# Kernel optimization log

Hardware: AMD Instinct MI355X
Metric: run time of the kernel (lower is better)

The kernel has to match this reference:

```python
import jax, jax.numpy as jnp
import numpy as np

N_NODES = 50000
N_EDGES = 1600000
IN_DIM, HID_DIM, OUT_DIM = 128, 256, 128


def setup_inputs() -> dict:
    key = jax.random.key(0)
    ks = jax.random.split(key, 8)
    x = jax.random.normal(ks[0], (N_NODES, IN_DIM), dtype=jnp.float32)
    edge_index = jax.random.randint(ks[1], (2, N_EDGES), 0, N_NODES, dtype=jnp.int64)
    s = 0.05
    # Layer 1: SAGEConv(IN_DIM -> HID_DIM); lin_l has bias, lin_r has no bias (PyG default)
    Wl1 = jax.random.normal(ks[2], (IN_DIM, HID_DIM), dtype=jnp.float32) * s
    bl1 = jnp.zeros((HID_DIM,), dtype=jnp.float32)
    Wr1 = jax.random.normal(ks[3], (IN_DIM, HID_DIM), dtype=jnp.float32) * s
    # Layer 2: SAGEConv(HID_DIM -> OUT_DIM)
    Wl2 = jax.random.normal(ks[4], (HID_DIM, OUT_DIM), dtype=jnp.float32) * s
    bl2 = jnp.zeros((OUT_DIM,), dtype=jnp.float32)
    Wr2 = jax.random.normal(ks[5], (HID_DIM, OUT_DIM), dtype=jnp.float32) * s
    return {"x": x, "edge_index": edge_index, "Wl1": Wl1, "bl1": bl1, "Wr1": Wr1,
            "Wl2": Wl2, "bl2": bl2, "Wr2": Wr2}


def _sage_conv(x, src, dst, Wl, bl, Wr, n_nodes):
    # mean aggregation of source-node features at destination nodes
    agg = jax.ops.segment_sum(x[src], dst, num_segments=n_nodes)  # [N, d_in]
    deg = jax.ops.segment_sum(jnp.ones_like(dst, dtype=x.dtype), dst, num_segments=n_nodes)
    mean = agg / jnp.maximum(deg, 1.0)[:, None]
    # out = lin_l(mean) + lin_r(x)
    return mean @ Wl + bl + x @ Wr


def reference(x, edge_index, Wl1, bl1, Wr1, Wl2, bl2, Wr2):
    src, dst = edge_index[0], edge_index[1]
    n = x.shape[0]
    h = _sage_conv(x, src, dst, Wl1, bl1, Wr1, n)
    h = jax.nn.relu(h)  # dropout is identity in eval mode
    out = _sage_conv(h, src, dst, Wl2, bl2, Wr2, n)
    return out
```

## Files before the change

kernel.cpp:

```cpp
#include <hip/hip_runtime.h>


#define IN_DIM 128
#define HID_DIM 256
#define OUT_DIM 128

#define EPB 8192
#define EPT 8
#define NBMAX 784
#define BCAP 4096

typedef unsigned short u16;
typedef unsigned int u32;
typedef unsigned char u8;
typedef __attribute__((ext_vector_type(8))) short short8;
typedef __attribute__((ext_vector_type(4))) float float4v;
typedef __attribute__((ext_vector_type(2))) float float2v;

#if defined(__has_builtin)
#if __has_builtin(__builtin_amdgcn_cvt_pk_f32_fp8) && \
    __has_builtin(__builtin_amdgcn_cvt_pk_fp8_f32)
#define HAVE_HW_FP8 1
#endif
#endif

static __device__ __forceinline__ u16 f2bf(float f) {
    u32 u = __builtin_bit_cast(u32, f);
    u = (u + 0x7fffu + ((u >> 16) & 1u)) >> 16;
    return (u16)u;
}
static __device__ __forceinline__ float bf2f(u32 lo16) {
    return __builtin_bit_cast(float, lo16 << 16);
}

#if !defined(HAVE_HW_FP8)
static __device__ __forceinline__ float fp8_dec1(u32 v) {
    u32 s = (v & 0x80u) << 24;
    u32 e = (v >> 3) & 0xFu;
    u32 m = v & 7u;
    float mag = e ? __builtin_bit_cast(float, ((e + 120u) << 23) | (m << 20))
                  : (float)m * 0x1p-9f;
    return __builtin_bit_cast(float, __builtin_bit_cast(u32, mag) | s);
}
static __device__ __forceinline__ u32 fp8_enc1(float f) {
    u32 u = __builtin_bit_cast(u32, f);
    u32 s = (u >> 24) & 0x80u;
    float af = fabsf(f);
    if (af > 448.f) af = 448.f;
    u32 a = __builtin_bit_cast(u32, af);
    int e = (int)((a >> 23) & 0xFF) - 127;
    u32 q;
    if (af < 0x1p-10f) q = 0;
    else if (e < -6) {
        q = (u32)__builtin_rintf(af * 512.f);
    } else {
        u32 m = a & 0x7FFFFFu;
        u32 r = m >> 20;
        u32 rem = m & 0xFFFFFu;
        if (rem > 0x80000u || (rem == 0x80000u && (r & 1u))) r++;
        u32 ee = (u32)(e + 7);
        if (r == 8u) { r = 0; ee++; }
        if (ee >= 16u) { ee = 15u; r = 6u; }
        q = (ee << 3) | r;
    }
    return s | q;
}
#endif

template <bool HI>
static __device__ __forceinline__ float2v fp8pk2f(u32 w) {
#if defined(HAVE_HW_FP8)
    return __builtin_amdgcn_cvt_pk_f32_fp8(w, HI);
#else
    float2v r;
    u32 b0 = HI ? ((w >> 16) & 0xFFu) : (w & 0xFFu);
    u32 b1 = HI ? (w >> 24) : ((w >> 8) & 0xFFu);
    r.x = fp8_dec1(b0);
    r.y = fp8_dec1(b1);
    return r;
#endif
}
template <bool HI>
static __device__ __forceinline__ u32 f2fp8pk(float a, float b, u32 old) {
#if defined(HAVE_HW_FP8)
    return (u32)__builtin_amdgcn_cvt_pk_fp8_f32(a, b, (int)old, HI);
#else
    u32 pk = fp8_enc1(a) | (fp8_enc1(b) << 8);
    return HI ? ((old & 0x0000FFFFu) | (pk << 16))
              : ((old & 0xFFFF0000u) | pk);
#endif
}
static __device__ __forceinline__ u8 f2fp8_1(float v) {
    return (u8)(f2fp8pk<false>(v, v, 0u) & 0xFFu);
}


__global__ __launch_bounds__(1024) void prep_part(
    const int* __restrict__ src, const int* __restrict__ dst, int n_edges,
    int nb, int nchunk, int* __restrict__ gcur, u32* __restrict__ pairs,
    const float* __restrict__ x, u16* __restrict__ xb, u32* __restrict__ xq,
    const float* __restrict__ Wl1, const float* __restrict__ Wr1,
    const float* __restrict__ Wl2, const float* __restrict__ Wr2,
    u16* __restrict__ WTl1, u16* __restrict__ WTr1,
    u16* __restrict__ WTl2, u16* __restrict__ WTr2, int n4, int xblocks) {
    __shared__ int h[NBMAX];
    __shared__ int curs[NBMAX];
    int b = blockIdx.x;
    int t = threadIdx.x;
    if (b < nchunk) {
        for (int i = t; i < nb; i += 1024) h[i] = 0;
        __syncthreads();
        int base = b * EPB;
        int dv[EPT], sv[EPT];
        bool on[EPT];
#pragma unroll
        for (int j = 0; j < EPT; j++) {
            int i = base + j * 1024 + t;
            on[j] = i < n_edges;
            if (on[j]) {
                dv[j] = dst[i];
                sv[j] = src[i];
                atomicAdd(&h[dv[j] >> 6], 1);
            }
        }
        __syncthreads();
        for (int i = t; i < nb; i += 1024) {
            int c = h[i];
            curs[i] = (c > 0) ? (i * BCAP + atomicAdd(&gcur[i], c)) : 0;
        }
        __syncthreads();
#pragma unroll
        for (int j = 0; j < EPT; j++) {
            if (on[j]) {
                int pos = atomicAdd(&curs[dv[j] >> 6], 1);
                pairs[pos] = ((u32)(dv[j] & 63) << 16) | (u32)sv[j];
            }
        }
        return;
    }
    if (b < nchunk + xblocks) {
        int i = (b - nchunk) * 1024 + t;
        if (i < n4) {
            float4 v = *(const float4*)(x + (size_t)i * 4);
            uint2 o;
            o.x = (u32)f2bf(v.x) | ((u32)f2bf(v.y) << 16);
            o.y = (u32)f2bf(v.z) | ((u32)f2bf(v.w) << 16);
            *(uint2*)(xb + (size_t)i * 4) = o;
            u32 q = f2fp8pk<false>(v.x, v.y, 0u);
            q = f2fp8pk<true>(v.z, v.w, q);
            xq[i] = q;
        }
        return;
    }
    int j = (b - nchunk - xblocks) * 1024 + t;
    if (j >= 4 * 32768) return;
    int seg = j >> 15;
    int r = j & 32767;
    if (seg == 0) WTl1[r] = f2bf(Wl1[(size_t)(r & 127) * 256 + (r >> 7)]);
    else if (seg == 1) WTr1[r] = f2bf(Wr1[(size_t)(r & 127) * 256 + (r >> 7)]);
    else if (seg == 2) WTl2[r] = f2bf(Wl2[(size_t)(r & 255) * 128 + (r >> 8)]);
    else WTr2[r] = f2bf(Wr2[(size_t)(r & 255) * 128 + (r >> 8)]);
}


__global__ __launch_bounds__(1024) void bucket_scatter(
    const u32* __restrict__ pairs, const int* __restrict__ gcur,
    int n_nodes,
    int* __restrict__ offs, int* __restrict__ degs,
    float* __restrict__ inv_deg, int* __restrict__ csr) {
    int b = blockIdx.x;
    int t = threadIdx.x;
    int beg = b * BCAP;
    int cnt_b = gcur[b];
    if (cnt_b > BCAP) cnt_b = BCAP;
    int end = beg + cnt_b;
    __shared__ u32 pbuf[BCAP];
    __shared__ int cnt[64];
    __shared__ int cur[64];
    if (t < 64) cnt[t] = 0;
    __syncthreads();
    for (int i = beg + t; i < end; i += 1024) {
        u32 pr = pairs[i];
        pbuf[i - beg] = pr;
        atomicAdd(&cnt[(pr >> 16) & 63], 1);
    }
    __syncthreads();
    if (t < 64) {
        int v = cnt[t];
        int incl = v;
#pragma unroll
        for (int off = 1; off < 64; off <<= 1) {
            int u = __shfl_up(incl, off, 64);
            if (t >= off) incl += u;
        }
        int o = beg + incl - v;
        int node = b * 64 + t;
        if (node < n_nodes) {
            offs[node] = o;
            degs[node] = v;
            inv_deg[node] = 1.0f / (float)(v > 0 ? v : 1);
        }
        cur[t] = o;
    }
    __syncthreads();
    for (int i = t; i < cnt_b; i += 1024) {
        u32 pr = pbuf[i];
        int p = atomicAdd(&cur[(pr >> 16) & 63], 1);
        csr[p] = (int)(pr & 0xffffu);
    }
}


__global__ __launch_bounds__(256) void agg_fp8(
    const u32* __restrict__ feat, const int* __restrict__ offs,
    const int* __restrict__ degs, const int* __restrict__ csr,
    const float* __restrict__ inv_deg, int n_nodes,
    u16* __restrict__ out_bf, float* __restrict__ out_f) {
    int wave = threadIdx.x >> 6;
    int lane = threadIdx.x & 63;
    int node = blockIdx.x * 4 + wave;
    if (node >= n_nodes) return;
    int beg = offs[node];
    int end = beg + degs[node];
    int half = lane >> 5, l32 = lane & 31;
    float a0 = 0.f, a1 = 0.f, a2 = 0.f, a3 = 0.f;
    int i = beg;
    for (; i + 32 <= end; i += 32) {
        u32 w[16];
#pragma unroll
        for (int j = 0; j < 16; j++) {
            int s = csr[i + 2 * j + half];
            w[j] = feat[(size_t)s * 32 + l32];
        }
#pragma unroll
        for (int j = 0; j < 16; j++) {
            float2v lo = fp8pk2f<false>(w[j]);
            float2v hi = fp8pk2f<true>(w[j]);
            a0 += lo.x;
            a1 += lo.y;
            a2 += hi.x;
            a3 += hi.y;
        }
    }
    if (i + 16 <= end) {
        u32 w[8];
#pragma unroll
        for (int j = 0; j < 8; j++) {
            int s = csr[i + 2 * j + half];
            w[j] = feat[(size_t)s * 32 + l32];
        }
#pragma unroll
        for (int j = 0; j < 8; j++) {
            float2v lo = fp8pk2f<false>(w[j]);
            float2v hi = fp8pk2f<true>(w[j]);
            a0 += lo.x;
            a1 += lo.y;
            a2 += hi.x;
            a3 += hi.y;
        }
        i += 16;
    }
    if (i + 8 <= end) {
        u32 w[4];
#pragma unroll
        for (int j = 0; j < 4; j++) {
            int s = csr[i + 2 * j + half];
            w[j] = feat[(size_t)s * 32 + l32];
        }
#pragma unroll
        for (int j = 0; j < 4; j++) {
            float2v lo = fp8pk2f<false>(w[j]);
            float2v hi = fp8pk2f<true>(w[j]);
            a0 += lo.x;
            a1 += lo.y;
            a2 += hi.x;
            a3 += hi.y;
        }
        i += 8;
    }
    for (; i < end; i += 2) {
        bool on = (i + half) < end;
        u32 w = 0;
        if (on) {
            int s = csr[i + half];
            w = feat[(size_t)s * 32 + l32];
        }
        float2v lo = fp8pk2f<false>(w);
        float2v hi = fp8pk2f<true>(w);
        if (on) {
            a0 += lo.x;
            a1 += lo.y;
            a2 += hi.x;
            a3 += hi.y;
        }
    }
    a0 += __shfl_xor(a0, 32);
    a1 += __shfl_xor(a1, 32);
    a2 += __shfl_xor(a2, 32);
    a3 += __shfl_xor(a3, 32);
    float inv = inv_deg[node];
    a0 *= inv;
    a1 *= inv;
    a2 *= inv;
    a3 *= inv;
    if (half == 0) {
        if (out_bf) {
            uint2 o;
            o.x = (u32)f2bf(a0) | ((u32)f2bf(a1) << 16);
            o.y = (u32)f2bf(a2) | ((u32)f2bf(a3) << 16);
            *(uint2*)(out_bf + (size_t)node * 128 + l32 * 4) = o;
        } else {
            float4* q = (float4*)(out_f + (size_t)node * 128 + l32 * 4);
            float4 o = *q;
            o.x += a0;
            o.y += a1;
            o.z += a2;
            o.w += a3;
            *q = o;
        }
    }
}


__global__ __launch_bounds__(256) void gemm_l1(
    const u16* __restrict__ A1, const u16* __restrict__ A2,
    const u16* __restrict__ BT1, const u16* __restrict__ BT2,
    const float* __restrict__ bias, u16* __restrict__ out_bf, int M) {
    const int K = IN_DIM, N = HID_DIM;
    __shared__ u16 Bs[128 * 128];
    int t = threadIdx.x;
    int colbase = blockIdx.x * 128;
    int lane = t & 63, wave = t >> 6, quad = lane >> 4, l16 = lane & 15;
    int row_base = blockIdx.y * 128 + wave * 32;
    float4v zero = {0.f, 0.f, 0.f, 0.f};
    float4v acc[2][8];
#pragma unroll
    for (int mi = 0; mi < 2; mi++)
#pragma unroll
        for (int ni = 0; ni < 8; ni++) acc[mi][ni] = zero;

    for (int mat = 0; mat < 2; mat++) {
        if (mat) __syncthreads();
        const u16* BT = mat ? BT2 : BT1;
        for (int c = t; c < 2048; c += 256) {
            int n = c >> 4;
            int e = (c & 15) * 8;
            int es = (e + n * 8) & 127;
            *(uint4*)&Bs[n * 128 + es] =
                *(const uint4*)(BT + (size_t)(colbase + n) * K + e);
        }
        __syncthreads();
        const u16* A = mat ? A2 : A1;
#pragma unroll
        for (int ks = 0; ks < 4; ks++) {
            int k = ks * 32 + quad * 8;
            short8 af[2] = {{0, 0, 0, 0, 0, 0, 0, 0}, {0, 0, 0, 0, 0, 0, 0, 0}};
#pragma unroll
            for (int mi = 0; mi < 2; mi++) {
                int m = row_base + mi * 16 + l16;
                if (m < M) af[mi] = *(const short8*)(A + (size_t)m * K + k);
            }
#pragma unroll
            for (int ni = 0; ni < 8; ni++) {
                int nn = ni * 16 + l16;
                int es = (k + nn * 8) & 127;
                short8 bfr = *(const short8*)&Bs[nn * 128 + es];
                acc[0][ni] = __builtin_amdgcn_mfma_f32_16x16x32_bf16(
                    af[0], bfr, acc[0][ni], 0, 0, 0);
                acc[1][ni] = __builtin_amdgcn_mfma_f32_16x16x32_bf16(
                    af[1], bfr, acc[1][ni], 0, 0, 0);
            }
        }
    }
#pragma unroll
    for (int mi = 0; mi < 2; mi++)
#pragma unroll
        for (int r = 0; r < 4; r++) {
            int row = row_base + mi * 16 + quad * 4 + r;
            if (row >= M) continue;
#pragma unroll
            for (int ni = 0; ni < 8; ni++) {
                int col = colbase + ni * 16 + l16;
                float v = acc[mi][ni][r] + bias[col];
                v = fmaxf(v, 0.f);
                out_bf[(size_t)row * N + col] = f2bf(v);
            }
        }
}

__global__ __launch_bounds__(256) void gemm_l2(
    const u16* __restrict__ A, const u16* __restrict__ BT1,
    const u16* __restrict__ BT2, const float* __restrict__ bias2,
    u8* __restrict__ out1_q, float* __restrict__ out2_f, int M) {
    const int K = HID_DIM, N = OUT_DIM;
    __shared__ u16 Bs[2][128 * 128];
    int t = threadIdx.x;
    int lane = t & 63, wave = t >> 6, quad = lane >> 4, l16 = lane & 15;
    int row_base = blockIdx.y * 128 + wave * 32;
    float4v zero = {0.f, 0.f, 0.f, 0.f};
    float4v acc1[2][8], acc2[2][8];
#pragma unroll
    for (int mi = 0; mi < 2; mi++)
#pragma unroll
        for (int ni = 0; ni < 8; ni++) {
            acc1[mi][ni] = zero;
            acc2[mi][ni] = zero;
        }

    for (int kc = 0; kc < 2; kc++) {
        if (kc) __syncthreads();
#pragma unroll
        for (int mat = 0; mat < 2; mat++) {
            const u16* BT = mat ? BT2 : BT1;
            for (int c = t; c < 2048; c += 256) {
                int n = c >> 4;
                int e = (c & 15) * 8;
                int es = (e + n * 8) & 127;
                *(uint4*)&Bs[mat][n * 128 + es] =
                    *(const uint4*)(BT + (size_t)n * K + kc * 128 + e);
            }
        }
        __syncthreads();
#pragma unroll
        for (int ks = 0; ks < 4; ks++) {
            int k = ks * 32 + quad * 8;
            int gk = kc * 128 + k;
            short8 af[2] = {{0, 0, 0, 0, 0, 0, 0, 0}, {0, 0, 0, 0, 0, 0, 0, 0}};
#pragma unroll
            for (int mi = 0; mi < 2; mi++) {
                int m = row_base + mi * 16 + l16;
                if (m < M) af[mi] = *(const short8*)(A + (size_t)m * K + gk);
            }
#pragma unroll
            for (int ni = 0; ni < 8; ni++) {
                int nn = ni * 16 + l16;
                int es = (k + nn * 8) & 127;
                short8 b1 = *(const short8*)&Bs[0][nn * 128 + es];
                short8 b2 = *(const short8*)&Bs[1][nn * 128 + es];
                acc1[0][ni] = __builtin_amdgcn_mfma_f32_16x16x32_bf16(
                    af[0], b1, acc1[0][ni], 0, 0, 0);
                acc1[1][ni] = __builtin_amdgcn_mfma_f32_16x16x32_bf16(
                    af[1], b1, acc1[1][ni], 0, 0, 0);
                acc2[0][ni] = __builtin_amdgcn_mfma_f32_16x16x32_bf16(
                    af[0], b2, acc2[0][ni], 0, 0, 0);
                acc2[1][ni] = __builtin_amdgcn_mfma_f32_16x16x32_bf16(
                    af[1], b2, acc2[1][ni], 0, 0, 0);
            }
        }
    }
#pragma unroll
    for (int mi = 0; mi < 2; mi++)
#pragma unroll
        for (int r = 0; r < 4; r++) {
            int row = row_base + mi * 16 + quad * 4 + r;
            if (row >= M) continue;
#pragma unroll
            for (int ni = 0; ni < 8; ni++) {
                int col = ni * 16 + l16;
                out1_q[(size_t)row * N + col] = f2fp8_1(acc1[mi][ni][r]);
                out2_f[(size_t)row * N + col] = acc2[mi][ni][r] + bias2[col];
            }
        }
}


extern "C" void kernel_launch(void* const* d_in, const int* in_sizes, int n_in,
                              void* d_out, int out_size, void* d_ws, size_t ws_size,
                              hipStream_t stream) {
    const float* x   = (const float*)d_in[0];
    const int*  eidx = (const int*)d_in[1];
    const float* Wl1 = (const float*)d_in[2];
    const float* bl1 = (const float*)d_in[3];
    const float* Wr1 = (const float*)d_in[4];
    const float* Wl2 = (const float*)d_in[5];
    const float* bl2 = (const float*)d_in[6];
    const float* Wr2 = (const float*)d_in[7];

    int n_nodes = in_sizes[0] / IN_DIM;
    int n_edges = in_sizes[1] / 2;
    const int* src = eidx;
    const int* dst = eidx + n_edges;
    int nb = (n_nodes + 63) / 64;
    int nchunk = (n_edges + EPB - 1) / EPB;

    char* p = (char*)d_ws;
    auto alloc = [&](size_t bytes) {
        void* q = (void*)p;
        p += (bytes + 255) & ~(size_t)255;
        return q;
    };
    int*   gcur    = (int*)alloc((size_t)nb * 4);
    int*   offs    = (int*)alloc((size_t)n_nodes * 4);
    int*   degs    = (int*)alloc((size_t)n_nodes * 4);
    float* inv_deg = (float*)alloc((size_t)n_nodes * 4);
    u32*   pairs   = (u32*)alloc(((size_t)nb * BCAP + 8192) * 4);
    int*   csr     = (int*)alloc(((size_t)nb * BCAP + 8192) * 4);
    u16*   xb      = (u16*)alloc((size_t)n_nodes * IN_DIM * 2);
    u32*   xq      = (u32*)alloc((size_t)n_nodes * IN_DIM);
    u16*   mean1b  = (u16*)alloc((size_t)n_nodes * IN_DIM * 2);
    u16*   hb      = (u16*)alloc((size_t)n_nodes * HID_DIM * 2);
    u8*    pbq     = (u8*)alloc((size_t)n_nodes * OUT_DIM);
    u16*   WTl1b   = (u16*)alloc((size_t)IN_DIM * HID_DIM * 2);
    u16*   WTr1b   = (u16*)alloc((size_t)IN_DIM * HID_DIM * 2);
    u16*   WTl2b   = (u16*)alloc((size_t)HID_DIM * OUT_DIM * 2);
    u16*   WTr2b   = (u16*)alloc((size_t)HID_DIM * OUT_DIM * 2);

    int n4 = n_nodes * IN_DIM / 4;
    int xblocks = (n4 + 1023) / 1024;
    int wblocks = (4 * 32768 + 1023) / 1024;

    hipMemsetAsync(gcur, 0, (size_t)nb * 4, stream);

    prep_part<<<nchunk + xblocks + wblocks, 1024, 0, stream>>>(
        src, dst, n_edges, nb, nchunk, gcur, pairs, x, xb, xq,
        Wl1, Wr1, Wl2, Wr2, WTl1b, WTr1b, WTl2b, WTr2b, n4, xblocks);

    bucket_scatter<<<nb, 1024, 0, stream>>>(pairs, gcur, n_nodes, offs, degs,
                                            inv_deg, csr);

    int gx = (n_nodes + 127) / 128;

    agg_fp8<<<(n_nodes + 3) / 4, 256, 0, stream>>>(xq, offs, degs, csr,
                                                   inv_deg, n_nodes, mean1b,
                                                   nullptr);
    {
        dim3 g(HID_DIM / 128, gx);
        gemm_l1<<<g, 256, 0, stream>>>(mean1b, xb, WTl1b, WTr1b, bl1, hb,
                                       n_nodes);
    }

    {
        dim3 g(1, gx);
        gemm_l2<<<g, 256, 0, stream>>>(hb, WTl2b, WTr2b, bl2, pbq,
                                       (float*)d_out, n_nodes);
    }
    agg_fp8<<<(n_nodes + 3) / 4, 256, 0, stream>>>((const u32*)pbq, offs, degs,
                                                   csr, inv_deg, n_nodes,
                                                   nullptr, (float*)d_out);
}
```

Before: 242.4 us.

## Fuse layer-1 mean aggregation into bucket scatter kernel and shrink CSR to u16

```diff
diff --git a/kernel.cpp b/kernel.cpp
--- a/kernel.cpp
+++ b/kernel.cpp
@@ -163,25 +163,27 @@
 }
 
 
-__global__ __launch_bounds__(1024) void bucket_scatter(
+__global__ __launch_bounds__(1024) void bucket_agg(
     const u32* __restrict__ pairs, const int* __restrict__ gcur,
-    int n_nodes,
+    const u32* __restrict__ feat, int n_nodes,
     int* __restrict__ offs, int* __restrict__ degs,
-    float* __restrict__ inv_deg, int* __restrict__ csr) {
+    float* __restrict__ inv_deg, u16* __restrict__ csr,
+    u16* __restrict__ out_bf) {
     int b = blockIdx.x;
     int t = threadIdx.x;
     int beg = b * BCAP;
     int cnt_b = gcur[b];
     if (cnt_b > BCAP) cnt_b = BCAP;
-    int end = beg + cnt_b;
     __shared__ u32 pbuf[BCAP];
+    __shared__ u16 csrl[BCAP];
     __shared__ int cnt[64];
     __shared__ int cur[64];
+    __shared__ int soff[64];
     if (t < 64) cnt[t] = 0;
     __syncthreads();
-    for (int i = beg + t; i < end; i += 1024) {
-        u32 pr = pairs[i];
-        pbuf[i - beg] = pr;
+    for (int i = t; i < cnt_b; i += 1024) {
+        u32 pr = pairs[beg + i];
+        pbuf[i] = pr;
         atomicAdd(&cnt[(pr >> 16) & 63], 1);
     }
     __syncthreads();
@@ -193,29 +195,128 @@
             int u = __shfl_up(incl, off, 64);
             if (t >= off) incl += u;
         }
-        int o = beg + incl - v;
+        int o = incl - v;
+        soff[t] = o;
+        cur[t] = o;
         int node = b * 64 + t;
         if (node < n_nodes) {
-            offs[node] = o;
+            offs[node] = beg + o;
             degs[node] = v;
             inv_deg[node] = 1.0f / (float)(v > 0 ? v : 1);
         }
-        cur[t] = o;
     }
     __syncthreads();
     for (int i = t; i < cnt_b; i += 1024) {
         u32 pr = pbuf[i];
         int p = atomicAdd(&cur[(pr >> 16) & 63], 1);
-        csr[p] = (int)(pr & 0xffffu);
+        u16 s = (u16)(pr & 0xffffu);
+        csrl[p] = s;
+        csr[beg + p] = s;
+    }
+    __syncthreads();
+    int wave = t >> 6, lane = t & 63;
+    int half = lane >> 5, l32 = lane & 31;
+#pragma unroll 1
+    for (int q = 0; q < 4; q++) {
+        int ln = wave * 4 + q;
+        int node = b * 64 + ln;
+        int s0 = soff[ln];
+        int deg = cnt[ln];
+        float a0 = 0.f, a1 = 0.f, a2 = 0.f, a3 = 0.f;
+        int i = 0;
+        for (; i + 32 <= deg; i += 32) {
+            u32 w[16];
+#pragma unroll
+            for (int j = 0; j < 16; j++) {
+                int s = csrl[s0 + i + 2 * j + half];
+                w[j] = feat[(size_t)s * 32 + l32];
+            }
+#pragma unroll
+            for (int j = 0; j < 16; j++) {
+                float2v lo = fp8pk2f<false>(w[j]);
+                float2v hi = fp8pk2f<true>(w[j]);
+                a0 += lo.x;
+                a1 += lo.y;
+                a2 += hi.x;
+                a3 += hi.y;
+            }
+        }
+        if (i + 16 <= deg) {
+            u32 w[8];
+#pragma unroll
+            for (int j = 0; j < 8; j++) {
+                int s = csrl[s0 + i + 2 * j + half];
+                w[j] = feat[(size_t)s * 32 + l32];
+            }
+#pragma unroll
+            for (int j = 0; j < 8; j++) {
+                float2v lo = fp8pk2f<false>(w[j]);
+                float2v hi = fp8pk2f<true>(w[j]);
+                a0 += lo.x;
+                a1 += lo.y;
+                a2 += hi.x;
+                a3 += hi.y;
+            }
+            i += 16;
+        }
+        if (i + 8 <= deg) {
+            u32 w[4];
+#pragma unroll
+            for (int j = 0; j < 4; j++) {
+                int s = csrl[s0 + i + 2 * j + half];
+                w[j] = feat[(size_t)s * 32 + l32];
+            }
+#pragma unroll
+            for (int j = 0; j < 4; j++) {
+                float2v lo = fp8pk2f<false>(w[j]);
+                float2v hi = fp8pk2f<true>(w[j]);
+                a0 += lo.x;
+                a1 += lo.y;
+                a2 += hi.x;
+                a3 += hi.y;
+            }
+            i += 8;
+        }
+        for (; i < deg; i += 2) {
+            bool on = (i + half) < deg;
+            u32 w = 0;
+            if (on) {
+                int s = csrl[s0 + i + half];
+                w = feat[(size_t)s * 32 + l32];
+            }
+            float2v lo = fp8pk2f<false>(w);
+            float2v hi = fp8pk2f<true>(w);
+            if (on) {
+                a0 += lo.x;
+                a1 += lo.y;
+                a2 += hi.x;
+                a3 += hi.y;
+            }
+        }
+        a0 += __shfl_xor(a0, 32);
+        a1 += __shfl_xor(a1, 32);
+        a2 += __shfl_xor(a2, 32);
+        a3 += __shfl_xor(a3, 32);
+        float inv = 1.0f / (float)(deg > 0 ? deg : 1);
+        a0 *= inv;
+        a1 *= inv;
+        a2 *= inv;
+        a3 *= inv;
+        if (half == 0 && node < n_nodes) {
+            uint2 o;
+            o.x = (u32)f2bf(a0) | ((u32)f2bf(a1) << 16);
+            o.y = (u32)f2bf(a2) | ((u32)f2bf(a3) << 16);
+            *(uint2*)(out_bf + (size_t)node * 128 + l32 * 4) = o;
+        }
     }
 }
 
 
 __global__ __launch_bounds__(256) void agg_fp8(
     const u32* __restrict__ feat, const int* __restrict__ offs,
-    const int* __restrict__ degs, const int* __restrict__ csr,
+    const int* __restrict__ degs, const u16* __restrict__ csr,
     const float* __restrict__ inv_deg, int n_nodes,
-    u16* __restrict__ out_bf, float* __restrict__ out_f) {
+    float* __restrict__ out_f) {
     int wave = threadIdx.x >> 6;
     int lane = threadIdx.x & 63;
     int node = blockIdx.x * 4 + wave;
@@ -304,20 +405,13 @@
     a2 *= inv;
     a3 *= inv;
     if (half == 0) {
-        if (out_bf) {
-            uint2 o;
-            o.x = (u32)f2bf(a0) | ((u32)f2bf(a1) << 16);
-            o.y = (u32)f2bf(a2) | ((u32)f2bf(a3) << 16);
-            *(uint2*)(out_bf + (size_t)node * 128 + l32 * 4) = o;
-        } else {
-            float4* q = (float4*)(out_f + (size_t)node * 128 + l32 * 4);
-            float4 o = *q;
-            o.x += a0;
-            o.y += a1;
-            o.z += a2;
-            o.w += a3;
-            *q = o;
-        }
+        float4* q = (float4*)(out_f + (size_t)node * 128 + l32 * 4);
+        float4 o = *q;
+        o.x += a0;
+        o.y += a1;
+        o.z += a2;
+        o.w += a3;
+        *q = o;
     }
 }
 
@@ -494,7 +588,7 @@
     int*   degs    = (int*)alloc((size_t)n_nodes * 4);
     float* inv_deg = (float*)alloc((size_t)n_nodes * 4);
     u32*   pairs   = (u32*)alloc(((size_t)nb * BCAP + 8192) * 4);
-    int*   csr     = (int*)alloc(((size_t)nb * BCAP + 8192) * 4);
+    u16*   csr     = (u16*)alloc(((size_t)nb * BCAP + 8192) * 2);
     u16*   xb      = (u16*)alloc((size_t)n_nodes * IN_DIM * 2);
     u32*   xq      = (u32*)alloc((size_t)n_nodes * IN_DIM);
     u16*   mean1b  = (u16*)alloc((size_t)n_nodes * IN_DIM * 2);
@@ -515,14 +609,11 @@
         src, dst, n_edges, nb, nchunk, gcur, pairs, x, xb, xq,
         Wl1, Wr1, Wl2, Wr2, WTl1b, WTr1b, WTl2b, WTr2b, n4, xblocks);
 
-    bucket_scatter<<<nb, 1024, 0, stream>>>(pairs, gcur, n_nodes, offs, degs,
-                                            inv_deg, csr);
+    bucket_agg<<<nb, 1024, 0, stream>>>(pairs, gcur, xq, n_nodes, offs, degs,
+                                        inv_deg, csr, mean1b);
 
     int gx = (n_nodes + 127) / 128;
 
-    agg_fp8<<<(n_nodes + 3) / 4, 256, 0, stream>>>(xq, offs, degs, csr,
-                                                   inv_deg, n_nodes, mean1b,
-                                                   nullptr);
     {
         dim3 g(HID_DIM / 128, gx);
         gemm_l1<<<g, 256, 0, stream>>>(mean1b, xb, WTl1b, WTr1b, bl1, hb,
@@ -536,5 +627,5 @@
     }
     agg_fp8<<<(n_nodes + 3) / 4, 256, 0, stream>>>((const u32*)pbq, offs, degs,
                                                    csr, inv_deg, n_nodes,
-                                                   nullptr, (float*)d_out);
-}
+                                                   (float*)d_out);
+}
```

New measurement: 236.5 us. 1.03x faster.

## Fuse first-half aggregation into bucket scatter and split gathers into 64-column passes

Applied to the files above, without the earlier changes.

```diff
diff --git a/kernel.cpp b/kernel.cpp
--- a/kernel.cpp
+++ b/kernel.cpp
@@ -16,6 +16,7 @@
 typedef __attribute__((ext_vector_type(8))) short short8;
 typedef __attribute__((ext_vector_type(4))) float float4v;
 typedef __attribute__((ext_vector_type(2))) float float2v;
+typedef __attribute__((ext_vector_type(2))) u32 uint2v;
 
 #if defined(__has_builtin)
 #if __has_builtin(__builtin_amdgcn_cvt_pk_f32_fp8) && \
@@ -28,9 +29,6 @@
     u32 u = __builtin_bit_cast(u32, f);
     u = (u + 0x7fffu + ((u >> 16) & 1u)) >> 16;
     return (u16)u;
-}
-static __device__ __forceinline__ float bf2f(u32 lo16) {
-    return __builtin_bit_cast(float, lo16 << 16);
 }
 
 #if !defined(HAVE_HW_FP8)
@@ -133,7 +131,8 @@
         for (int j = 0; j < EPT; j++) {
             if (on[j]) {
                 int pos = atomicAdd(&curs[dv[j] >> 6], 1);
-                pairs[pos] = ((u32)(dv[j] & 63) << 16) | (u32)sv[j];
+                __builtin_nontemporal_store(
+                    ((u32)(dv[j] & 63) << 16) | (u32)sv[j], &pairs[pos]);
             }
         }
         return;
@@ -162,26 +161,92 @@
     else WTr2[r] = f2bf(Wr2[(size_t)(r & 255) * 128 + (r >> 8)]);
 }
 
-
-__global__ __launch_bounds__(1024) void bucket_scatter(
+#define GATHER_LADDER(IDXOP)                                           \
+    {                                                                  \
+        int i = 0;                                                     \
+        for (; i + 32 <= degmx; i += 32) {                             \
+            u32 w[16];                                                 \
+            _Pragma("unroll") for (int j = 0; j < 16; j++) {           \
+                int idx = i + 2 * j + q16;                             \
+                if (idx < deg) {                                       \
+                    int s = (int)(IDXOP(idx));                         \
+                    w[j] = fp[(size_t)s * 32];                         \
+                } else w[j] = 0;                                       \
+            }                                                          \
+            _Pragma("unroll") for (int j = 0; j < 16; j++) {           \
+                float2v lo = fp8pk2f<false>(w[j]);                     \
+                float2v hi = fp8pk2f<true>(w[j]);                      \
+                a0 += lo.x; a1 += lo.y; a2 += hi.x; a3 += hi.y;        \
+            }                                                          \
+        }                                                              \
+        if (i + 16 <= degmx) {                                         \
+            u32 w[8];                                                  \
+            _Pragma("unroll") for (int j = 0; j < 8; j++) {            \
+                int idx = i + 2 * j + q16;                             \
+                if (idx < deg) {                                       \
+                    int s = (int)(IDXOP(idx));                         \
+                    w[j] = fp[(size_t)s * 32];                         \
+                } else w[j] = 0;                                       \
+            }                                                          \
+            _Pragma("unroll") for (int j = 0; j < 8; j++) {            \
+                float2v lo = fp8pk2f<false>(w[j]);                     \
+                float2v hi = fp8pk2f<true>(w[j]);                      \
+                a0 += lo.x; a1 += lo.y; a2 += hi.x; a3 += hi.y;        \
+            }                                                          \
+            i += 16;                                                   \
+        }                                                              \
+        if (i + 8 <= degmx) {                                          \
+            u32 w[4];                                                  \
+            _Pragma("unroll") for (int j = 0; j < 4; j++) {            \
+                int idx = i + 2 * j + q16;                             \
+                if (idx < deg) {                                       \
+                    int s = (int)(IDXOP(idx));                         \
+                    w[j] = fp[(size_t)s * 32];                         \
+                } else w[j] = 0;                                       \
+            }                                                          \
+            _Pragma("unroll") for (int j = 0; j < 4; j++) {            \
+                float2v lo = fp8pk2f<false>(w[j]);                     \
+                float2v hi = fp8pk2f<true>(w[j]);                      \
+                a0 += lo.x; a1 += lo.y; a2 += hi.x; a3 += hi.y;        \
+            }                                                          \
+            i += 8;                                                    \
+        }                                                              \
+        for (; i < degmx; i += 2) {                                    \
+            int idx = i + q16;                                         \
+            u32 w = 0;                                                 \
+            if (idx < deg) {                                           \
+                int s = (int)(IDXOP(idx));                             \
+                w = fp[(size_t)s * 32];                                \
+            }                                                          \
+            float2v lo = fp8pk2f<false>(w);                            \
+            float2v hi = fp8pk2f<true>(w);                             \
+            if (idx < deg) {                                           \
+                a0 += lo.x; a1 += lo.y; a2 += hi.x; a3 += hi.y;        \
+            }                                                          \
+        }                                                              \
+    }
+
+
+__global__ __launch_bounds__(1024) void bucket_agg(
     const u32* __restrict__ pairs, const int* __restrict__ gcur,
-    int n_nodes,
+    const u32* __restrict__ feat, int n_nodes,
     int* __restrict__ offs, int* __restrict__ degs,
-    float* __restrict__ inv_deg, int* __restrict__ csr) {
+    u16* __restrict__ csr, u16* __restrict__ out_bf) {
     int b = blockIdx.x;
     int t = threadIdx.x;
     int beg = b * BCAP;
     int cnt_b = gcur[b];
     if (cnt_b > BCAP) cnt_b = BCAP;
-    int end = beg + cnt_b;
     __shared__ u32 pbuf[BCAP];
+    __shared__ u16 csrl[BCAP];
     __shared__ int cnt[64];
     __shared__ int cur[64];
+    __shared__ int soff[64];
     if (t < 64) cnt[t] = 0;
     __syncthreads();
-    for (int i = beg + t; i < end; i += 1024) {
-        u32 pr = pairs[i];
-        pbuf[i - beg] = pr;
+    for (int i = t; i < cnt_b; i += 1024) {
+        u32 pr = __builtin_nontemporal_load(&pairs[beg + i]);
+        pbuf[i] = pr;
         atomicAdd(&cnt[(pr >> 16) & 63], 1);
     }
     __syncthreads();
@@ -193,130 +258,99 @@
             int u = __shfl_up(incl, off, 64);
             if (t >= off) incl += u;
         }
-        int o = beg + incl - v;
+        int o = incl - v;
+        soff[t] = o;
+        cur[t] = o;
         int node = b * 64 + t;
         if (node < n_nodes) {
-            offs[node] = o;
+            offs[node] = beg + o;
             degs[node] = v;
-            inv_deg[node] = 1.0f / (float)(v > 0 ? v : 1);
-        }
-        cur[t] = o;
+        }
     }
     __syncthreads();
     for (int i = t; i < cnt_b; i += 1024) {
         u32 pr = pbuf[i];
         int p = atomicAdd(&cur[(pr >> 16) & 63], 1);
-        csr[p] = (int)(pr & 0xffffu);
-    }
-}
-
-
-__global__ __launch_bounds__(256) void agg_fp8(
+        u16 s = (u16)(pr & 0xffffu);
+        csrl[p] = s;
+        __builtin_nontemporal_store(s, &csr[beg + p]);
+    }
+    __syncthreads();
+    int wave = t >> 6, lane = t & 63;
+    int h = lane >> 5, q16 = (lane >> 4) & 1, l16 = lane & 15;
+    const u32* fp = feat + l16;
+#pragma unroll 1
+    for (int r = 0; r < 2; r++) {
+        int ln = (wave + r * 16) * 2 + h;
+        int node = b * 64 + ln;
+        int s0 = soff[ln];
+        int deg = cnt[ln];
+        int dother = __shfl_xor(deg, 32);
+        int degmx = deg > dother ? deg : dother;
+        float a0 = 0.f, a1 = 0.f, a2 = 0.f, a3 = 0.f;
+#define IDX_LDS(idx) csrl[s0 + (idx)]
+        GATHER_LADDER(IDX_LDS)
+#undef IDX_LDS
+        a0 += __shfl_xor(a0, 16);
+        a1 += __shfl_xor(a1, 16);
+        a2 += __shfl_xor(a2, 16);
+        a3 += __shfl_xor(a3, 16);
+        float inv = 1.0f / (float)(deg > 0 ? deg : 1);
+        if (q16 == 0 && node < n_nodes) {
+            uint2v o;
+            o.x = (u32)f2bf(a0 * inv) | ((u32)f2bf(a1 * inv) << 16);
+            o.y = (u32)f2bf(a2 * inv) | ((u32)f2bf(a3 * inv) << 16);
+            __builtin_nontemporal_store(
+                o, (uint2v*)(out_bf + (size_t)node * 128 + l16 * 4));
+        }
+    }
+}
+
+
+__global__ __launch_bounds__(256) void agg64(
     const u32* __restrict__ feat, const int* __restrict__ offs,
-    const int* __restrict__ degs, const int* __restrict__ csr,
-    const float* __restrict__ inv_deg, int n_nodes,
-    u16* __restrict__ out_bf, float* __restrict__ out_f) {
+    const int* __restrict__ degs, const u16* __restrict__ csr,
+    int n_nodes, int pass, u16* __restrict__ out_bf,
+    float* __restrict__ out_f) {
     int wave = threadIdx.x >> 6;
     int lane = threadIdx.x & 63;
-    int node = blockIdx.x * 4 + wave;
-    if (node >= n_nodes) return;
-    int beg = offs[node];
-    int end = beg + degs[node];
-    int half = lane >> 5, l32 = lane & 31;
+    int h = lane >> 5, q16 = (lane >> 4) & 1, l16 = lane & 15;
+    int np = blockIdx.x * 8 + wave * 2 + h;
+    bool act = np < n_nodes;
+    int deg = act ? degs[np] : 0;
+    int s0 = act ? offs[np] : 0;
+    int dother = __shfl_xor(deg, 32);
+    int degmx = deg > dother ? deg : dother;
+    const u32* fp = feat + pass * 16 + l16;
     float a0 = 0.f, a1 = 0.f, a2 = 0.f, a3 = 0.f;
-    int i = beg;
-    for (; i + 32 <= end; i += 32) {
-        u32 w[16];
-#pragma unroll
-        for (int j = 0; j < 16; j++) {
-            int s = csr[i + 2 * j + half];
-            w[j] = feat[(size_t)s * 32 + l32];
-        }
-#pragma unroll
-        for (int j = 0; j < 16; j++) {
-            float2v lo = fp8pk2f<false>(w[j]);
-            float2v hi = fp8pk2f<true>(w[j]);
-            a0 += lo.x;
-            a1 += lo.y;
-            a2 += hi.x;
-            a3 += hi.y;
-        }
-    }
-    if (i + 16 <= end) {
-        u32 w[8];
-#pragma unroll
-        for (int j = 0; j < 8; j++) {
-            int s = csr[i + 2 * j + half];
-            w[j] = feat[(size_t)s * 32 + l32];
-        }
-#pragma unroll
-        for (int j = 0; j < 8; j++) {
-            float2v lo = fp8pk2f<false>(w[j]);
-            float2v hi = fp8pk2f<true>(w[j]);
-            a0 += lo.x;
-            a1 += lo.y;
-            a2 += hi.x;
-            a3 += hi.y;
-        }
-        i += 16;
-    }
-    if (i + 8 <= end) {
-        u32 w[4];
-#pragma unroll
-        for (int j = 0; j < 4; j++) {
-            int s = csr[i + 2 * j + half];
-            w[j] = feat[(size_t)s * 32 + l32];
-        }
-#pragma unroll
-        for (int j = 0; j < 4; j++) {
-            float2v lo = fp8pk2f<false>(w[j]);
-            float2v hi = fp8pk2f<true>(w[j]);
-            a0 += lo.x;
-            a1 += lo.y;
-            a2 += hi.x;
-            a3 += hi.y;
-        }
-        i += 8;
-    }
-    for (; i < end; i += 2) {
-        bool on = (i + half) < end;
-        u32 w = 0;
-        if (on) {
-            int s = csr[i + half];
-            w = feat[(size_t)s * 32 + l32];
-        }
-        float2v lo = fp8pk2f<false>(w);
-        float2v hi = fp8pk2f<true>(w);
-        if (on) {
-            a0 += lo.x;
-            a1 += lo.y;
-            a2 += hi.x;
-            a3 += hi.y;
-        }
-    }
-    a0 += __shfl_xor(a0, 32);
-    a1 += __shfl_xor(a1, 32);
-    a2 += __shfl_xor(a2, 32);
-    a3 += __shfl_xor(a3, 32);
-    float inv = inv_deg[node];
+#define IDX_GL(idx) __builtin_nontemporal_load(&csr[s0 + (idx)])
+    GATHER_LADDER(IDX_GL)
+#undef IDX_GL
+    a0 += __shfl_xor(a0, 16);
+    a1 += __shfl_xor(a1, 16);
+    a2 += __shfl_xor(a2, 16);
+    a3 += __shfl_xor(a3, 16);
+    float inv = 1.0f / (float)(deg > 0 ? deg : 1);
     a0 *= inv;
     a1 *= inv;
     a2 *= inv;
     a3 *= inv;
-    if (half == 0) {
+    if (q16 == 0 && act) {
         if (out_bf) {
-            uint2 o;
+            uint2v o;
             o.x = (u32)f2bf(a0) | ((u32)f2bf(a1) << 16);
             o.y = (u32)f2bf(a2) | ((u32)f2bf(a3) << 16);
-            *(uint2*)(out_bf + (size_t)node * 128 + l32 * 4) = o;
+            __builtin_nontemporal_store(
+                o, (uint2v*)(out_bf + (size_t)np * 128 + pass * 64 + l16 * 4));
         } else {
-            float4* q = (float4*)(out_f + (size_t)node * 128 + l32 * 4);
-            float4 o = *q;
+            float4v* q =
+                (float4v*)(out_f + (size_t)np * 128 + pass * 64 + l16 * 4);
+            float4v o = __builtin_nontemporal_load(q);
             o.x += a0;
             o.y += a1;
             o.z += a2;
             o.w += a3;
-            *q = o;
+            __builtin_nontemporal_store(o, q);
         }
     }
 }
@@ -458,7 +492,9 @@
             for (int ni = 0; ni < 8; ni++) {
                 int col = ni * 16 + l16;
                 out1_q[(size_t)row * N + col] = f2fp8_1(acc1[mi][ni][r]);
-                out2_f[(size_t)row * N + col] = acc2[mi][ni][r] + bias2[col];
+                __builtin_nontemporal_store(
+                    acc2[mi][ni][r] + bias2[col],
+                    out2_f + (size_t)row * N + col);
             }
         }
 }
@@ -492,9 +528,8 @@
     int*   gcur    = (int*)alloc((size_t)nb * 4);
     int*   offs    = (int*)alloc((size_t)n_nodes * 4);
     int*   degs    = (int*)alloc((size_t)n_nodes * 4);
-    float* inv_deg = (float*)alloc((size_t)n_nodes * 4);
     u32*   pairs   = (u32*)alloc(((size_t)nb * BCAP + 8192) * 4);
-    int*   csr     = (int*)alloc(((size_t)nb * BCAP + 8192) * 4);
+    u16*   csr     = (u16*)alloc(((size_t)nb * BCAP + 8192) * 2);
     u16*   xb      = (u16*)alloc((size_t)n_nodes * IN_DIM * 2);
     u32*   xq      = (u32*)alloc((size_t)n_nodes * IN_DIM);
     u16*   mean1b  = (u16*)alloc((size_t)n_nodes * IN_DIM * 2);
@@ -515,14 +550,14 @@
         src, dst, n_edges, nb, nchunk, gcur, pairs, x, xb, xq,
         Wl1, Wr1, Wl2, Wr2, WTl1b, WTr1b, WTl2b, WTr2b, n4, xblocks);
 
-    bucket_scatter<<<nb, 1024, 0, stream>>>(pairs, gcur, n_nodes, offs, degs,
-                                            inv_deg, csr);
+    bucket_agg<<<nb, 1024, 0, stream>>>(pairs, gcur, xq, n_nodes, offs, degs,
+                                        csr, mean1b);
+    int agrid = (n_nodes + 7) / 8;
+    agg64<<<agrid, 256, 0, stream>>>(xq, offs, degs, csr, n_nodes, 1, mean1b,
+                                     nullptr);
 
     int gx = (n_nodes + 127) / 128;
 
-    agg_fp8<<<(n_nodes + 3) / 4, 256, 0, stream>>>(xq, offs, degs, csr,
-                                                   inv_deg, n_nodes, mean1b,
-                                                   nullptr);
     {
         dim3 g(HID_DIM / 128, gx);
         gemm_l1<<<g, 256, 0, stream>>>(mean1b, xb, WTl1b, WTr1b, bl1, hb,
@@ -534,7 +569,8 @@
         gemm_l2<<<g, 256, 0, stream>>>(hb, WTl2b, WTr2b, bl2, pbq,
                                        (float*)d_out, n_nodes);
     }
-    agg_fp8<<<(n_nodes + 3) / 4, 256, 0, stream>>>((const u32*)pbq, offs, degs,
-                                                   csr, inv_deg, n_nodes,
-                                                   nullptr, (float*)d_out);
-}
+    agg64<<<agrid, 256, 0, stream>>>((const u32*)pbq, offs, degs, csr, n_nodes,
+                                     0, nullptr, (float*)d_out);
+    agg64<<<agrid, 256, 0, stream>>>((const u32*)pbq, offs, degs, csr, n_nodes,
+                                     1, nullptr, (float*)d_out);
+}
```

New measurement: 378.4 us. +56.1%, slower.
